# Optimization experiments

Measured on AMD Instinct MI355X. Metric: run time of the kernel, lower is better.

## Reference

```python
import jax, jax.numpy as jnp
import numpy as np

B, S, D, H, WIN = 2, 2048, 1024, 16, 512
DK = D // H
NEG_INF = float('-inf')


def setup_inputs() -> dict:
    key = jax.random.key(0)
    ks = jax.random.split(key, 9)
    sc = 1.0 / np.sqrt(D)
    def w(k):
        return jax.random.normal(k, (D, D), jnp.float32) * sc
    def b(k):
        return jax.random.normal(k, (D,), jnp.float32) * 0.01
    return {
        'x': jax.random.normal(ks[0], (B, S, D), jnp.float32),
        'Wq_w': w(ks[1]), 'Wq_b': b(jax.random.fold_in(ks[1], 1)),
        'Wk_w': w(ks[2]), 'Wk_b': b(jax.random.fold_in(ks[2], 1)),
        'Wv_w': w(ks[3]), 'Wv_b': b(jax.random.fold_in(ks[3], 1)),
        'Wo_w': w(ks[4]), 'Wo_b': b(jax.random.fold_in(ks[4], 1)),
    }


def _sliding_window_softmax(scores):
    """Faithful port of _apply_sliding_window_attention.

    scores: [B, H, S, S]. seq_len is a multiple of WIN (padding_len == 0,
    which is the only case where the original torch code runs without a
    shape error). Reshape rows/cols into WIN-sized blocks, apply the full
    causal mask (viewed block-wise), softmax over the within-window key
    axis, reshape back. Rows whose entire window block is masked produce
    NaN in torch; here they are defined as 0 (safe softmax) so the
    reference is numerically usable.
    """
    b, h, s, _ = scores.shape
    nb = s // WIN
    causal = jnp.tril(jnp.ones((s, s), dtype=bool)).reshape(1, 1, nb, WIN, nb, WIN)
    sc = scores.reshape(b, h, nb, WIN, nb, WIN)
    sc = jnp.where(causal, sc, NEG_INF)
    m = jnp.max(sc, axis=-1, keepdims=True)
    e = jnp.exp(sc - jnp.where(jnp.isfinite(m), m, 0.0))
    e = jnp.where(causal, e, 0.0)
    denom = jnp.sum(e, axis=-1, keepdims=True)
    probs = e / jnp.where(denom == 0.0, 1.0, denom)
    return probs.reshape(b, h, s, s)


def reference(x, Wq_w, Wq_b, Wk_w, Wk_b, Wv_w, Wv_b, Wo_w, Wo_b):
    b, s, d = x.shape
    # torch nn.Linear: y = x @ W.T + b
    q = (x @ Wq_w.T + Wq_b).reshape(b, s, H, DK).transpose(0, 2, 1, 3)  # [B,H,S,DK]
    k = (x @ Wk_w.T + Wk_b).reshape(b, s, H, DK).transpose(0, 2, 1, 3)
    v = (x @ Wv_w.T + Wv_b).reshape(b, s, H, DK).transpose(0, 2, 1, 3)

    attn_scores = jnp.einsum('bhqd,bhkd->bhqk', q, k) / np.sqrt(DK)  # [B,H,S,S]
    if WIN < s:  # sliding-window branch (window softmax, as in the source)
        attn_scores = _sliding_window_softmax(attn_scores)
    # second, full-row softmax (the source applies softmax again)
    attn_probs = jax.nn.softmax(attn_scores, axis=-1)
    attn_out = jnp.einsum('bhqk,bhkd->bhqd', attn_probs, v)
    attn_out = attn_out.transpose(0, 2, 1, 3).reshape(b, s, d)
    return attn_out @ Wo_w.T + Wo_b
```

## Files before the change

kernel.cpp:

```cpp
#include <hip/hip_runtime.h>
#include <hip/hip_bf16.h>

typedef short v8s __attribute__((ext_vector_type(8)));
typedef float v4f __attribute__((ext_vector_type(4)));
typedef unsigned int v4u __attribute__((ext_vector_type(4)));
typedef unsigned int v2u __attribute__((ext_vector_type(2)));

#define DEV static __device__ __forceinline__
#define AS1 __attribute__((address_space(1)))
#define AS3 __attribute__((address_space(3)))

DEV float bf2f(unsigned short u){ unsigned int x=((unsigned int)u)<<16; float f; __builtin_memcpy(&f,&x,4); return f; }
DEV short f2bf(float f){ __hip_bfloat16 h=__float2bfloat16(f); short s; __builtin_memcpy(&s,&h,2); return s; }
DEV unsigned int f2bfu(float f){ unsigned int u; __builtin_memcpy(&u,&f,4); return (u + 0x7fffu + ((u>>16)&1u)) >> 16; }
DEV unsigned int pk2(float a, float b){ return f2bfu(a) | (f2bfu(b)<<16); }
DEV v4f mfma16(v8s a, v8s b, v4f c){ return __builtin_amdgcn_mfma_f32_16x16x32_bf16(a,b,c,0,0,0); }
DEV float fexp2(float x){
#if __has_builtin(__builtin_amdgcn_exp2f)
  return __builtin_amdgcn_exp2f(x);
#else
  float r; asm("v_exp_f32 %0, %1" : "=v"(r) : "v"(x)); return r;
#endif
}

__global__ __launch_bounds__(256) void convert_kernel(
    const float* __restrict__ x,  const float* __restrict__ Wq,
    const float* __restrict__ Wk, const float* __restrict__ Wv,
    short* __restrict__ xb, short* __restrict__ wqb,
    short* __restrict__ wkb, short* __restrict__ wvb)
{
  unsigned g = blockIdx.x*256u + threadIdx.x;
  const float* src; short* dst; unsigned off;
  if (g < 1048576u){ src=x;  dst=xb;  off=g; }
  else if (g < 1310720u){ src=Wq; dst=wqb; off=g-1048576u; }
  else if (g < 1572864u){ src=Wk; dst=wkb; off=g-1310720u; }
  else { src=Wv; dst=wvb; off=g-1572864u; }
  v4f f = *(const v4f*)(src + (size_t)off*4);
  v2u r; r[0]=pk2(f[0],f[1]); r[1]=pk2(f[2],f[3]);
  *(v2u*)(dst + (size_t)off*4) = r;
}

DEV void gemm_core16(const short* __restrict__ A, const short* __restrict__ Bmat,
                     int brow0, int bn0, int tid, short* As, short* Bs, v4f acc[4][4])
{
  const int l = tid & 63, w = tid >> 6;
  const int wr = (w>>1)*64, wc = (w&1)*64;
  const int row = tid>>2, p = tid&3;
  const int sw = (p^((row>>1)&3))*8;
  auto STAGE=[&](int kt,int buf){
    const short* a0 = A    + (size_t)(brow0+row   )*1024 + kt*32 + sw;
    const short* a1 = A    + (size_t)(brow0+row+64)*1024 + kt*32 + sw;
    const short* b0 = Bmat + (size_t)(bn0 +row   )*1024 + kt*32 + sw;
    const short* b1 = Bmat + (size_t)(bn0 +row+64)*1024 + kt*32 + sw;
    __builtin_amdgcn_global_load_lds((const AS1 void*)a0,(AS3 void*)(As+buf*4096+(size_t)tid*8),16,0,0);
    __builtin_amdgcn_global_load_lds((const AS1 void*)a1,(AS3 void*)(As+buf*4096+(size_t)(tid+256)*8),16,0,0);
    __builtin_amdgcn_global_load_lds((const AS1 void*)b0,(AS3 void*)(Bs+buf*4096+(size_t)tid*8),16,0,0);
    __builtin_amdgcn_global_load_lds((const AS1 void*)b1,(AS3 void*)(Bs+buf*4096+(size_t)(tid+256)*8),16,0,0);
  };
  STAGE(0,0);
  asm volatile("s_waitcnt vmcnt(0)" ::: "memory");
  __builtin_amdgcn_s_barrier();
  int cur=0;
  for (int kt=0; kt<32; ++kt){
    if (kt<31) STAGE(kt+1,cur^1);
    v8s af[4], bfr[4];
    #pragma unroll
    for (int m=0;m<4;++m){ int r=wr+m*16+(l&15); af[m]=*(const v8s*)&As[cur*4096+(r*4+((l>>4)^((r>>1)&3)))*8]; }
    #pragma unroll
    for (int n=0;n<4;++n){ int r=wc+n*16+(l&15); bfr[n]=*(const v8s*)&Bs[cur*4096+(r*4+((l>>4)^((r>>1)&3)))*8]; }
    #pragma unroll
    for (int m=0;m<4;++m)
      #pragma unroll
      for (int n=0;n<4;++n)
        acc[m][n]=mfma16(af[m],bfr[n],acc[m][n]);
    asm volatile("s_waitcnt vmcnt(0)" ::: "memory");
    __builtin_amdgcn_s_barrier();
    cur^=1;
  }
}

DEV void gemm_core_f32(const short* __restrict__ A, const float* __restrict__ B32,
                   int brow0, int bn0, int tid, short* As, short* Bs, v4f acc[4][4])
{
  const int l = tid & 63, w = tid >> 6;
  const int wr = (w>>1)*64, wc = (w&1)*64;
  for (int kt=0; kt<32; ++kt){
    v4u ra0, ra1, rb0, rb1;
    {
      int idx=tid;      int row=idx>>2, p=idx&3;
      ra0 = *(const v4u*)(A + (size_t)(brow0+row)*1024 + kt*32 + (p^((row>>1)&3))*8);
      idx=tid+256;      row=idx>>2; p=idx&3;
      ra1 = *(const v4u*)(A + (size_t)(brow0+row)*1024 + kt*32 + (p^((row>>1)&3))*8);
      idx=tid;          row=idx>>2; p=idx&3;
      {
        const float* s0 = B32 + (size_t)(bn0+row)*1024 + kt*32 + (p^((row>>1)&3))*8;
        v4f f0=*(const v4f*)s0, f1=*(const v4f*)(s0+4);
        rb0[0]=pk2(f0[0],f0[1]); rb0[1]=pk2(f0[2],f0[3]);
        rb0[2]=pk2(f1[0],f1[1]); rb0[3]=pk2(f1[2],f1[3]);
      }
      idx=tid+256;      row=idx>>2; p=idx&3;
      {
        const float* s1 = B32 + (size_t)(bn0+row)*1024 + kt*32 + (p^((row>>1)&3))*8;
        v4f f0=*(const v4f*)s1, f1=*(const v4f*)(s1+4);
        rb1[0]=pk2(f0[0],f0[1]); rb1[1]=pk2(f0[2],f0[3]);
        rb1[2]=pk2(f1[0],f1[1]); rb1[3]=pk2(f1[2],f1[3]);
      }
    }
    __syncthreads();
    *(v4u*)&As[(size_t)tid*8]       = ra0;
    *(v4u*)&As[(size_t)(tid+256)*8] = ra1;
    *(v4u*)&Bs[(size_t)tid*8]       = rb0;
    *(v4u*)&Bs[(size_t)(tid+256)*8] = rb1;
    __syncthreads();
    v8s af[4], bfr[4];
    #pragma unroll
    for (int m=0;m<4;++m){ int r=wr+m*16+(l&15); af[m]=*(const v8s*)&As[(r*4+((l>>4)^((r>>1)&3)))*8]; }
    #pragma unroll
    for (int n=0;n<4;++n){ int r=wc+n*16+(l&15); bfr[n]=*(const v8s*)&Bs[(r*4+((l>>4)^((r>>1)&3)))*8]; }
    #pragma unroll
    for (int m=0;m<4;++m)
      #pragma unroll
      for (int n=0;n<4;++n)
        acc[m][n]=mfma16(af[m],bfr[n],acc[m][n]);
  }
}

__global__ __launch_bounds__(256) void qkv_gemm(const short* __restrict__ xb,
    const short* __restrict__ wqb, const short* __restrict__ wkb, const short* __restrict__ wvb,
    const float* __restrict__ bq, const float* __restrict__ bk, const float* __restrict__ bv,
    short* __restrict__ qo, short* __restrict__ ko, short* __restrict__ vfo)
{
  __shared__ short As[8192], Bs[8192];
  const int tid=threadIdx.x, l=tid&63, w=tid>>6;
  const int bcol0=blockIdx.x*128, brow0=blockIdx.y*128;
  const int mat=bcol0>>10, n0=bcol0&1023;
  const short* Wm   = mat==0?wqb:(mat==1?wkb:wvb);
  const float* bias = mat==0?bq:(mat==1?bk:bv);
  v4f acc[4][4];
  v4f vz={0.f,0.f,0.f,0.f};
  #pragma unroll
  for(int m=0;m<4;++m)
    #pragma unroll
    for(int n=0;n<4;++n) acc[m][n]=vz;
  gemm_core16(xb, Wm, brow0, n0, tid, As, Bs, acc);
  const int wr=(w>>1)*64, wc=(w&1)*64;
  const float qscale = 0.18033688011112042f;
  #pragma unroll
  for(int m=0;m<4;++m)
  #pragma unroll
  for(int n=0;n<4;++n)
  #pragma unroll
  for(int r=0;r<4;++r){
    int row=brow0+wr+m*16+(l>>4)*4+r;
    int col=n0+wc+n*16+(l&15);
    float v=acc[m][n][r]+bias[col];
    int b=row>>11, s=row&2047, h=col>>6, dk=col&63;
    int bh=b*16+h;
    if(mat==0)      qo[((size_t)bh*2048+s)*64+dk]=f2bf(v*qscale);
    else if(mat==1) ko[((size_t)bh*2048+s)*64+dk]=f2bf(v);
    else{
      int kb=s>>9, c=(s>>5)&15, ki=s&31;
      int g2=(ki>>2)&3, j=(ki>>4)*4+(ki&3);
      int lane2=g2*16+(dk&15);
      vfo[((((size_t)bh*4+kb)*16+c)*4+(size_t)(dk>>4))*512 + lane2*8 + j]=f2bf(v);
    }
  }
}

__global__ __launch_bounds__(64) void vbsum_kernel(const short* __restrict__ vf, float* __restrict__ vbp)
{
  const int bh=blockIdx.x, kb=blockIdx.y, l=threadIdx.x;
  const short* base = vf + ((size_t)(bh*4+kb))*16*4*512;
  float acc[4]={0.f,0.f,0.f,0.f};
  #pragma unroll
  for(int c=0;c<16;++c)
    #pragma unroll
    for(int dt=0;dt<4;++dt){
      v8s vv=*(const v8s*)(base + ((size_t)(c*4+dt))*512 + l*8);
      float s=0.f;
      #pragma unroll
      for(int j=0;j<8;++j) s+=bf2f((unsigned short)vv[j]);
      acc[dt]+=s;
    }
  #pragma unroll
  for(int dt=0;dt<4;++dt){
    acc[dt]+=__shfl_xor(acc[dt],16);
    acc[dt]+=__shfl_xor(acc[dt],32);
  }
  if(l<16){
    #pragma unroll
    for(int dt=0;dt<4;++dt) vbp[(size_t)(bh*4+kb)*64 + dt*16 + l]=acc[dt];
  }
}

__global__ __launch_bounds__(256) void attn_kernel(
  const short* __restrict__ q, const short* __restrict__ k, const short* __restrict__ vf,
  const float* __restrict__ vbp, short* __restrict__ attn)
{
  __shared__ short kbuf[16384];
  __shared__ float d1buf[256];
  const int tid=threadIdx.x, l=tid&63, wv=tid>>6;
  const int bh=blockIdx.x, qt=31-blockIdx.y;
  const int qb=qt>>3;
  const int qrow0=qt*64+wv*16;
  const int g=l>>4, q16=l&15;
  const int b=bh>>4, h=bh&15;
  const int qglob=qrow0+q16;
  const int lrow=wv*16+q16;

  const short* qbase = q + (size_t)bh*2048*64;
  const short* kbase = k + (size_t)bh*2048*64;
  const short* qp = qbase + (size_t)(qrow0+q16)*64 + g*8;
  v8s qa0=*(const v8s*)qp, qa1=*(const v8s*)(qp+32);
  v4f vz={0.f,0.f,0.f,0.f};

  auto stage=[&](int kb2,int hb2){
    #pragma unroll
    for (int i=0;i<8;++i){
      int idx=i*256+tid, key=idx>>3, p=idx&7, pp=p^(key&7);
      const short* gp = kbase + (size_t)(kb2*512+hb2*256+key)*64 + pp*8;
      __builtin_amdgcn_global_load_lds((const AS1 void*)gp,
          (AS3 void*)((char*)kbuf + idx*16), 16, 0, 0);
    }
  };

#define QKE(CT, EV)                                                     \
  v4f EV;                                                               \
  { int krow=((CT)&15)*16+q16;                                          \
    int s0=g^(krow&7), s1=(g+4)^(krow&7);                               \
    v8s k0=*(const v8s*)&kbuf[(krow*8+s0)*8];                           \
    v8s k1=*(const v8s*)&kbuf[(krow*8+s1)*8];                           \
    v4f t=mfma16(k0,qa0,vz);                                            \
    v4f e4=mfma16(k1,qa1,t);                                            \
    _Pragma("unroll")                                                   \
    for (int r=0;r<4;++r){                                              \
      float s=e4[r];                                                    \
      if (diag && kb*512+(CT)*16+g*4+r > qglob) s=-1e38f;               \
      EV[r]=fexp2(s);                                                   \
    }                                                                   \
  }

  for (int kb=0; kb<=qb; ++kb){
    const bool diag=(kb==qb);
    const int tmaxw = diag ? ((qt&7)*4+wv) : 31;
    const int blkhi = diag ? ((qt&7)*4+3) : 31;
    float d1acc=0.f;
    stage(kb,0); __syncthreads();
    #pragma unroll
    for (int ct=0;ct<16;++ct) if (ct<=tmaxw){
      QKE(ct,ev)
      d1acc+=(ev[0]+ev[1])+(ev[2]+ev[3]);
    }
    __syncthreads();
    if (blkhi>=16){
      stage(kb,1); __syncthreads();
      #pragma unroll
      for (int ct=16;ct<32;++ct) if (ct<=tmaxw){
        QKE(ct,ev)
        d1acc+=(ev[0]+ev[1])+(ev[2]+ev[3]);
      }
      __syncthreads();
    }
    float d1=d1acc;
    d1+=__shfl_xor(d1,16); d1+=__shfl_xor(d1,32);
    if (l<16) d1buf[(wv*16+l)*4+kb]=1.44269504f/d1;
  }
  __syncthreads();

  v4f o[4];
  #pragma unroll
  for(int dt=0;dt<4;++dt) o[dt]=vz;
  float zacc=0.f;

#define CHUNK(C)                                                        \
  { QKE(2*(C),eA) QKE(2*(C)+1,eB)                                       \
    float w0=fexp2(eA[0]*d1i)-1.0f, w1=fexp2(eA[1]*d1i)-1.0f;           \
    float w2=fexp2(eA[2]*d1i)-1.0f, w3=fexp2(eA[3]*d1i)-1.0f;           \
    float w4=fexp2(eB[0]*d1i)-1.0f, w5=fexp2(eB[1]*d1i)-1.0f;           \
    float w6=fexp2(eB[2]*d1i)-1.0f, w7=fexp2(eB[3]*d1i)-1.0f;           \
    zacc+=((w0+w1)+(w2+w3))+((w4+w5)+(w6+w7));                          \
    union { v4u u; v8s s; } pa;                                         \
    pa.u[0]=pk2(w0,w1); pa.u[1]=pk2(w2,w3);                             \
    pa.u[2]=pk2(w4,w5); pa.u[3]=pk2(w6,w7);                             \
    const short* vfp = vf + ((((size_t)bh*4+kb)*16+(C))*4)*512 + l*8;   \
    _Pragma("unroll")                                                   \
    for (int dt=0;dt<4;++dt){                                           \
      v8s vfr=*(const v8s*)(vfp + (size_t)dt*512);                      \
      o[dt]=mfma16(pa.s,vfr,o[dt]);                                     \
    }                                                                   \
  }

  for (int kb=0; kb<=qb; ++kb){
    const bool diag=(kb==qb);
    const int tmaxw = diag ? ((qt&7)*4+wv) : 31;
    const int blkhi = diag ? ((qt&7)*4+3) : 31;
    const float d1i=d1buf[lrow*4+kb];
    stage(kb,0); __syncthreads();
    #pragma unroll
    for (int c=0;c<8;++c) if (2*c<=tmaxw) CHUNK(c)
    __syncthreads();
    if (blkhi>=16){
      stage(kb,1); __syncthreads();
      #pragma unroll
      for (int c=8;c<16;++c) if (2*c<=tmaxw) CHUNK(c)
      __syncthreads();
    }
  }
#undef CHUNK
#undef QKE

  float z=zacc;
  z+=__shfl_xor(z,16); z+=__shfl_xor(z,32);
  float base[4];
  #pragma unroll
  for (int dt=0;dt<4;++dt){
    float s=0.f;
    #pragma unroll
    for (int kk=0;kk<4;++kk) s+=vbp[(size_t)(bh*4+kk)*64 + dt*16 + q16];
    base[dt]=s;
  }
  #pragma unroll
  for (int r=0;r<4;++r){
    float zr=__shfl(z, g*4+r);
    float inv=1.0f/(2048.0f+zr);
    int rowi=qrow0+g*4+r;
    size_t obase=((size_t)b*2048+rowi)*1024 + h*64;
    #pragma unroll
    for (int dt=0;dt<4;++dt)
      attn[obase + dt*16 + q16] = f2bf((o[dt][r]+base[dt])*inv);
  }
}

__global__ __launch_bounds__(256) void oproj_gemm(const short* __restrict__ at,
    const float* __restrict__ Wo, const float* __restrict__ bo, float* __restrict__ out)
{
  __shared__ short As[4096], Bs[4096];
  const int tid=threadIdx.x, l=tid&63, w=tid>>6;
  const int bcol0=blockIdx.x*128, brow0=blockIdx.y*128;
  v4f acc[4][4];
  v4f vz={0.f,0.f,0.f,0.f};
  #pragma unroll
  for(int m=0;m<4;++m)
    #pragma unroll
    for(int n=0;n<4;++n) acc[m][n]=vz;
  gemm_core_f32(at, Wo, brow0, bcol0, tid, As, Bs, acc);
  const int wr=(w>>1)*64, wc=(w&1)*64;
  #pragma unroll
  for(int m=0;m<4;++m)
  #pragma unroll
  for(int n=0;n<4;++n)
  #pragma unroll
  for(int r=0;r<4;++r){
    int row=brow0+wr+m*16+(l>>4)*4+r;
    int col=bcol0+wc+n*16+(l&15);
    out[(size_t)row*1024+col]=acc[m][n][r]+bo[col];
  }
}

extern "C" void kernel_launch(void* const* d_in, const int* in_sizes, int n_in,
                              void* d_out, int out_size, void* d_ws, size_t ws_size,
                              hipStream_t stream)
{
  const float* x  =(const float*)d_in[0];
  const float* Wq =(const float*)d_in[1];
  const float* bq =(const float*)d_in[2];
  const float* Wk =(const float*)d_in[3];
  const float* bk =(const float*)d_in[4];
  const float* Wv =(const float*)d_in[5];
  const float* bv =(const float*)d_in[6];
  const float* Wo =(const float*)d_in[7];
  const float* bo =(const float*)d_in[8];
  float* out=(float*)d_out;
  char* ws=(char*)d_ws;
  short* xb_ws =(short*)(ws);
  short* at_ws =(short*)(ws);
  short* q_ws  =(short*)(ws + ((size_t)8<<20));
  short* k_ws  =(short*)(ws + ((size_t)16<<20));
  short* vf_ws =(short*)(ws + ((size_t)24<<20));
  char*  outb  =(char*)d_out;
  short* wqb   =(short*)(outb);
  short* wkb   =(short*)(outb + ((size_t)2<<20));
  short* wvb   =(short*)(outb + ((size_t)4<<20));
  float* vbp_ws=(float*)(outb + ((size_t)7<<20));

  convert_kernel<<<dim3(7168),256,0,stream>>>(x,Wq,Wk,Wv,xb_ws,wqb,wkb,wvb);
  qkv_gemm<<<dim3(24,32),256,0,stream>>>(xb_ws,wqb,wkb,wvb,bq,bk,bv,q_ws,k_ws,vf_ws);
  vbsum_kernel<<<dim3(32,4),64,0,stream>>>(vf_ws,vbp_ws);
  attn_kernel<<<dim3(32,32),256,0,stream>>>(q_ws,k_ws,vf_ws,vbp_ws,at_ws);
  oproj_gemm<<<dim3(8,32),256,0,stream>>>(at_ws,Wo,bo,out);
}
```

Before: 156.6 us.

## Pre-convert Wo to bf16, use async-LDS gemm core, widen vbsum, add MFMA priority

Adds a separate kernel that converts Wo to bf16 into the freed q workspace region after attention. The output projection then reuses the double-buffered global_load_lds bf16 GEMM core instead of the fp32-load-and-convert synchronous core. The V-block sum kernel now uses four waves per block with an LDS reduction. The attention kernel raises wave priority around its MFMA sequences. These changes trade an extra launch and an extra Wo round-trip for a faster o-proj main loop and better latency hiding.

```diff
diff --git a/kernel.cpp b/kernel.cpp
--- a/kernel.cpp
+++ b/kernel.cpp
@@ -35,6 +35,15 @@
   else if (g < 1310720u){ src=Wq; dst=wqb; off=g-1048576u; }
   else if (g < 1572864u){ src=Wk; dst=wkb; off=g-1310720u; }
   else { src=Wv; dst=wvb; off=g-1572864u; }
+  v4f f = *(const v4f*)(src + (size_t)off*4);
+  v2u r; r[0]=pk2(f[0],f[1]); r[1]=pk2(f[2],f[3]);
+  *(v2u*)(dst + (size_t)off*4) = r;
+}
+
+__global__ __launch_bounds__(256) void convertW_kernel(const float* __restrict__ src,
+                                                       short* __restrict__ dst)
+{
+  unsigned off = blockIdx.x*256u + threadIdx.x;
   v4f f = *(const v4f*)(src + (size_t)off*4);
   v2u r; r[0]=pk2(f[0],f[1]); r[1]=pk2(f[2],f[3]);
   *(v2u*)(dst + (size_t)off*4) = r;
@@ -79,52 +88,6 @@
   }
 }
 
-DEV void gemm_core_f32(const short* __restrict__ A, const float* __restrict__ B32,
-                   int brow0, int bn0, int tid, short* As, short* Bs, v4f acc[4][4])
-{
-  const int l = tid & 63, w = tid >> 6;
-  const int wr = (w>>1)*64, wc = (w&1)*64;
-  for (int kt=0; kt<32; ++kt){
-    v4u ra0, ra1, rb0, rb1;
-    {
-      int idx=tid;      int row=idx>>2, p=idx&3;
-      ra0 = *(const v4u*)(A + (size_t)(brow0+row)*1024 + kt*32 + (p^((row>>1)&3))*8);
-      idx=tid+256;      row=idx>>2; p=idx&3;
-      ra1 = *(const v4u*)(A + (size_t)(brow0+row)*1024 + kt*32 + (p^((row>>1)&3))*8);
-      idx=tid;          row=idx>>2; p=idx&3;
-      {
-        const float* s0 = B32 + (size_t)(bn0+row)*1024 + kt*32 + (p^((row>>1)&3))*8;
-        v4f f0=*(const v4f*)s0, f1=*(const v4f*)(s0+4);
-        rb0[0]=pk2(f0[0],f0[1]); rb0[1]=pk2(f0[2],f0[3]);
-        rb0[2]=pk2(f1[0],f1[1]); rb0[3]=pk2(f1[2],f1[3]);
-      }
-      idx=tid+256;      row=idx>>2; p=idx&3;
-      {
-        const float* s1 = B32 + (size_t)(bn0+row)*1024 + kt*32 + (p^((row>>1)&3))*8;
-        v4f f0=*(const v4f*)s1, f1=*(const v4f*)(s1+4);
-        rb1[0]=pk2(f0[0],f0[1]); rb1[1]=pk2(f0[2],f0[3]);
-        rb1[2]=pk2(f1[0],f1[1]); rb1[3]=pk2(f1[2],f1[3]);
-      }
-    }
-    __syncthreads();
-    *(v4u*)&As[(size_t)tid*8]       = ra0;
-    *(v4u*)&As[(size_t)(tid+256)*8] = ra1;
-    *(v4u*)&Bs[(size_t)tid*8]       = rb0;
-    *(v4u*)&Bs[(size_t)(tid+256)*8] = rb1;
-    __syncthreads();
-    v8s af[4], bfr[4];
-    #pragma unroll
-    for (int m=0;m<4;++m){ int r=wr+m*16+(l&15); af[m]=*(const v8s*)&As[(r*4+((l>>4)^((r>>1)&3)))*8]; }
-    #pragma unroll
-    for (int n=0;n<4;++n){ int r=wc+n*16+(l&15); bfr[n]=*(const v8s*)&Bs[(r*4+((l>>4)^((r>>1)&3)))*8]; }
-    #pragma unroll
-    for (int m=0;m<4;++m)
-      #pragma unroll
-      for (int n=0;n<4;++n)
-        acc[m][n]=mfma16(af[m],bfr[n],acc[m][n]);
-  }
-}
-
 __global__ __launch_bounds__(256) void qkv_gemm(const short* __restrict__ xb,
     const short* __restrict__ wqb, const short* __restrict__ wkb, const short* __restrict__ wvb,
     const float* __restrict__ bq, const float* __restrict__ bk, const float* __restrict__ bv,
@@ -167,13 +130,15 @@
   }
 }
 
-__global__ __launch_bounds__(64) void vbsum_kernel(const short* __restrict__ vf, float* __restrict__ vbp)
-{
-  const int bh=blockIdx.x, kb=blockIdx.y, l=threadIdx.x;
+__global__ __launch_bounds__(256) void vbsum_kernel(const short* __restrict__ vf, float* __restrict__ vbp)
+{
+  __shared__ float red[4][4][16];
+  const int bh=blockIdx.x, kb=blockIdx.y, tid=threadIdx.x, wv=tid>>6, l=tid&63;
   const short* base = vf + ((size_t)(bh*4+kb))*16*4*512;
   float acc[4]={0.f,0.f,0.f,0.f};
   #pragma unroll
-  for(int c=0;c<16;++c)
+  for(int cc=0;cc<4;++cc){
+    int c=wv*4+cc;
     #pragma unroll
     for(int dt=0;dt<4;++dt){
       v8s vv=*(const v8s*)(base + ((size_t)(c*4+dt))*512 + l*8);
@@ -182,6 +147,7 @@
       for(int j=0;j<8;++j) s+=bf2f((unsigned short)vv[j]);
       acc[dt]+=s;
     }
+  }
   #pragma unroll
   for(int dt=0;dt<4;++dt){
     acc[dt]+=__shfl_xor(acc[dt],16);
@@ -189,7 +155,13 @@
   }
   if(l<16){
     #pragma unroll
-    for(int dt=0;dt<4;++dt) vbp[(size_t)(bh*4+kb)*64 + dt*16 + l]=acc[dt];
+    for(int dt=0;dt<4;++dt) red[wv][dt][l]=acc[dt];
+  }
+  __syncthreads();
+  if(tid<64){
+    int dt=tid>>4, d=tid&15;
+    float s=(red[0][dt][d]+red[1][dt][d])+(red[2][dt][d]+red[3][dt][d]);
+    vbp[(size_t)(bh*4+kb)*64 + dt*16 + d]=s;
   }
 }
 
@@ -230,8 +202,10 @@
     int s0=g^(krow&7), s1=(g+4)^(krow&7);                               \
     v8s k0=*(const v8s*)&kbuf[(krow*8+s0)*8];                           \
     v8s k1=*(const v8s*)&kbuf[(krow*8+s1)*8];                           \
+    __builtin_amdgcn_s_setprio(1);                                      \
     v4f t=mfma16(k0,qa0,vz);                                            \
     v4f e4=mfma16(k1,qa1,t);                                            \
+    __builtin_amdgcn_s_setprio(0);                                      \
     _Pragma("unroll")                                                   \
     for (int r=0;r<4;++r){                                              \
       float s=e4[r];                                                    \
@@ -283,11 +257,13 @@
     pa.u[0]=pk2(w0,w1); pa.u[1]=pk2(w2,w3);                             \
     pa.u[2]=pk2(w4,w5); pa.u[3]=pk2(w6,w7);                             \
     const short* vfp = vf + ((((size_t)bh*4+kb)*16+(C))*4)*512 + l*8;   \
+    __builtin_amdgcn_s_setprio(1);                                      \
     _Pragma("unroll")                                                   \
     for (int dt=0;dt<4;++dt){                                           \
       v8s vfr=*(const v8s*)(vfp + (size_t)dt*512);                      \
       o[dt]=mfma16(pa.s,vfr,o[dt]);                                     \
     }                                                                   \
+    __builtin_amdgcn_s_setprio(0);                                      \
   }
 
   for (int kb=0; kb<=qb; ++kb){
@@ -332,9 +308,9 @@
 }
 
 __global__ __launch_bounds__(256) void oproj_gemm(const short* __restrict__ at,
-    const float* __restrict__ Wo, const float* __restrict__ bo, float* __restrict__ out)
-{
-  __shared__ short As[4096], Bs[4096];
+    const short* __restrict__ wob, const float* __restrict__ bo, float* __restrict__ out)
+{
+  __shared__ short As[8192], Bs[8192];
   const int tid=threadIdx.x, l=tid&63, w=tid>>6;
   const int bcol0=blockIdx.x*128, brow0=blockIdx.y*128;
   v4f acc[4][4];
@@ -343,7 +319,7 @@
   for(int m=0;m<4;++m)
     #pragma unroll
     for(int n=0;n<4;++n) acc[m][n]=vz;
-  gemm_core_f32(at, Wo, brow0, bcol0, tid, As, Bs, acc);
+  gemm_core16(at, wob, brow0, bcol0, tid, As, Bs, acc);
   const int wr=(w>>1)*64, wc=(w&1)*64;
   #pragma unroll
   for(int m=0;m<4;++m)
@@ -375,6 +351,7 @@
   short* xb_ws =(short*)(ws);
   short* at_ws =(short*)(ws);
   short* q_ws  =(short*)(ws + ((size_t)8<<20));
+  short* wob_ws=(short*)(ws + ((size_t)8<<20));
   short* k_ws  =(short*)(ws + ((size_t)16<<20));
   short* vf_ws =(short*)(ws + ((size_t)24<<20));
   char*  outb  =(char*)d_out;
@@ -385,7 +362,8 @@
 
   convert_kernel<<<dim3(7168),256,0,stream>>>(x,Wq,Wk,Wv,xb_ws,wqb,wkb,wvb);
   qkv_gemm<<<dim3(24,32),256,0,stream>>>(xb_ws,wqb,wkb,wvb,bq,bk,bv,q_ws,k_ws,vf_ws);
-  vbsum_kernel<<<dim3(32,4),64,0,stream>>>(vf_ws,vbp_ws);
+  vbsum_kernel<<<dim3(32,4),256,0,stream>>>(vf_ws,vbp_ws);
   attn_kernel<<<dim3(32,32),256,0,stream>>>(q_ws,k_ws,vf_ws,vbp_ws,at_ws);
-  oproj_gemm<<<dim3(8,32),256,0,stream>>>(at_ws,Wo,bo,out);
-}
+  convertW_kernel<<<dim3(1024),256,0,stream>>>(Wo,wob_ws);
+  oproj_gemm<<<dim3(8,32),256,0,stream>>>(at_ws,wob_ws,bo,out);
+}
```

Result: faster. 152.1 us (-2.9%).
